# Optimization experiments

Measured on AMD Instinct MI355X. Metric: run time of the kernel, lower is better.

The kernel has to match this reference:

```python
import jax, jax.numpy as jnp
import numpy as np

B = 1_000_000
H = 64
TARGET = 0.62562059 * 10.0  # self.target * scale
# GRN constants from NETC_high.__init__
A1, A2, B1C, B2C, K, NEXP, S, SCALE = 1.0, 1.0, 0.2, 0.2, 1.1, 2, 0.5, 10.0


def setup_inputs() -> dict:
    key = jax.random.key(0)
    ks = jax.random.split(key, 10)
    def xavier(k, shape):
        fan_in, fan_out = shape[1], shape[0]
        std = (2.0 / (fan_in + fan_out)) ** 0.5
        return std * jax.random.normal(k, shape, dtype=jnp.float32)
    return {
        "x": jax.random.uniform(ks[0], (B,), dtype=jnp.float32) * 10.0,
        "y": jax.random.uniform(ks[1], (B,), dtype=jnp.float32) * 10.0,
        "e_x": 0.1 * jax.random.normal(ks[2], (B,), dtype=jnp.float32),
        "e_y": 0.1 * jax.random.normal(ks[3], (B,), dtype=jnp.float32),
        "W1": xavier(ks[4], (H, 2)),
        "b1": jnp.zeros((H,), dtype=jnp.float32),
        "W2": xavier(ks[5], (H, H)),
        "b2": jnp.zeros((H,), dtype=jnp.float32),
        "W3": xavier(ks[6], (1, H)),
        "b3": jnp.zeros((1,), dtype=jnp.float32),
    }


def _mlp(z, W1, b1, W2, b2, W3, b3):
    # ControlNet.function: Linear->ReLU->Linear->ReLU->Linear
    h = jax.nn.relu(z @ W1.T + b1)
    h = jax.nn.relu(h @ W2.T + b2)
    return h @ W3.T + b3  # [*, 1]


def _control(inp, W1, b1, W2, b2, W3, b3):
    # ControlNet.forward: u(x) - u(target)
    tgt = jnp.full((1, 2), TARGET, dtype=inp.dtype)
    return _mlp(inp, W1, b1, W2, b2, W3, b3) - _mlp(tgt, W1, b1, W2, b2, W3, b3)


def reference(x, y, e_x, e_y, W1, b1, W2, b2, W3, b3):
    inp = jnp.stack([x + e_x, y + e_y], axis=-1)  # [B, 2]
    u = _control(inp, W1, b1, W2, b2, W3, b3)[:, 0]  # [B]
    xs = x / SCALE
    ys = y / SCALE
    s2 = S ** NEXP
    hx = xs ** NEXP / (s2 + xs ** NEXP)   # Hill activation in x
    hy = ys ** NEXP / (s2 + ys ** NEXP)
    gx = s2 / (s2 + xs ** NEXP)           # Hill repression by x
    gy = s2 / (s2 + ys ** NEXP)
    dx = SCALE * (A1 * hx + B1C * gy - K * xs + u * hx)
    dy = SCALE * (A2 * hy + B2C * gx - K * ys)
    return (dx, dy, -dx, -dy)
```

## Files before the change

kernel.cpp:

```cpp
#include <hip/hip_runtime.h>

#define BTOT 1000000

typedef _Float16 f16;
typedef f16 f16x2 __attribute__((ext_vector_type(2)));
typedef f16 f16x8 __attribute__((ext_vector_type(8)));
typedef float f32x2 __attribute__((ext_vector_type(2)));
typedef float f32x4 __attribute__((ext_vector_type(4)));

#define WS_BFRAG 16
#define WS_W1A   8208
#define WS_W1B   10256
#define WS_B1P   12304
#define WS_W3V   14352
#define WS_B2V   15376

template<int CTRL>
__device__ __forceinline__ float dpp_add(float v) {
    int pv = __builtin_amdgcn_update_dpp(0, __builtin_bit_cast(int, v),
                                         CTRL, 0xF, 0xF, true);
    return v + __builtin_bit_cast(float, pv);
}
__device__ __forceinline__ float row_reduce16(float p) {
    p = dpp_add<0x128>(p);
    p = dpp_add<0x124>(p);
    p = dpp_add<0x122>(p);
    p = dpp_add<0x121>(p);
    return p;
}

__global__ __launch_bounds__(256) void setup_kernel(
    const float* __restrict__ W1, const float* __restrict__ b1,
    const float* __restrict__ W2, const float* __restrict__ b2,
    const float* __restrict__ W3, unsigned char* __restrict__ ws)
{
    const int tid  = threadIdx.x;
    const int quad = (tid & 63) >> 4;
    const int nl   = tid & 15;

    __shared__ float w2s[64 * 65];
    __shared__ float h1s[64];
    __shared__ float part[4 * 64];

    const float4* W2v = (const float4*)W2;
    #pragma unroll
    for (int r = 0; r < 4; ++r) {
        int idx = r * 256 + tid;
        float4 f = W2v[idx];
        int g = idx * 4, row = g >> 6, col = g & 63;
        float* p = &w2s[row * 65 + col];
        p[0] = f.x; p[1] = f.y; p[2] = f.z; p[3] = f.w;
    }
    const float T = 6.2562059f;
    if (tid < 64)
        h1s[tid] = fmaxf(0.f, W1[2 * tid] * T + W1[2 * tid + 1] * T + b1[tid]);
    __syncthreads();

    {
        int r = tid & 63, kq = tid >> 6;
        float p = 0.f;
        #pragma unroll
        for (int k = 0; k < 16; ++k)
            p = fmaf(w2s[r * 65 + kq * 16 + k], h1s[kq * 16 + k], p);
        part[kq * 64 + r] = p;
    }
    __syncthreads();
    if (tid < 64) {
        float h2 = b2[tid] + part[tid] + part[64 + tid] + part[128 + tid] + part[192 + tid];
        float pr = fmaxf(0.f, h2) * W3[tid];
        #pragma unroll
        for (int m = 1; m < 64; m <<= 1) pr += __shfl_xor(pr, m, 64);
        if (tid == 0) *(float*)ws = pr;
    }

    if (tid < 64) {
        f16x8* bfragT = (f16x8*)(ws + WS_BFRAG);
        #pragma unroll
        for (int n = 0; n < 4; ++n)
            #pragma unroll
            for (int ks = 0; ks < 2; ++ks) {
                f16x8 f;
                #pragma unroll
                for (int j = 0; j < 8; ++j)
                    f[j] = (f16)w2s[(n * 16 + nl) * 65 + ks * 32 + quad * 8 + j];
                bfragT[(n * 2 + ks) * 64 + tid] = f;
            }
        f16x2* w1aT = (f16x2*)(ws + WS_W1A);
        f16x2* w1bT = (f16x2*)(ws + WS_W1B);
        f16x2* b1pT = (f16x2*)(ws + WS_B1P);
        #pragma unroll
        for (int i = 0; i < 8; ++i) {
            int kk = (i < 4) ? (quad * 8 + 2 * i) : (32 + quad * 8 + 2 * (i - 4));
            w1aT[i * 64 + tid] = f16x2{(f16)W1[2 * kk],     (f16)W1[2 * kk + 2]};
            w1bT[i * 64 + tid] = f16x2{(f16)W1[2 * kk + 1], (f16)W1[2 * kk + 3]};
            b1pT[i * 64 + tid] = f16x2{(f16)b1[kk],         (f16)b1[kk + 1]};
        }
        float* w3vT = (float*)(ws + WS_W3V);
        float* b2vT = (float*)(ws + WS_B2V);
        #pragma unroll
        for (int n = 0; n < 4; ++n) {
            w3vT[n * 64 + tid] = W3[n * 16 + nl];
            b2vT[n * 64 + tid] = b2[n * 16 + nl];
        }
    }
}

__global__ __launch_bounds__(256, 4) void netc_kernel(
    const float* __restrict__ x,  const float* __restrict__ y,
    const float* __restrict__ ex, const float* __restrict__ ey,
    const unsigned char* __restrict__ ws,
    float* __restrict__ out)
{
    const int tid  = threadIdx.x;
    const int lane = tid & 63;
    const int wv   = tid >> 6;
    const int quad = lane >> 4;
    const int nl   = lane & 15;

    const float u_tgt = *(const float*)ws;
    const float one_minus_ut = 1.0f - u_tgt;
    const f16x8* bfragT = (const f16x8*)(ws + WS_BFRAG);
    f16x8 bfrag[4][2];
    #pragma unroll
    for (int n = 0; n < 4; ++n)
        #pragma unroll
        for (int ks = 0; ks < 2; ++ks)
            bfrag[n][ks] = bfragT[(n * 2 + ks) * 64 + lane];
    const f16x2* w1aT = (const f16x2*)(ws + WS_W1A);
    const f16x2* w1bT = (const f16x2*)(ws + WS_W1B);
    const f16x2* b1pT = (const f16x2*)(ws + WS_B1P);
    f16x2 w1a[8], w1b[8], b1p[8];
    #pragma unroll
    for (int i = 0; i < 8; ++i) {
        w1a[i] = w1aT[i * 64 + lane];
        w1b[i] = w1bT[i * 64 + lane];
        b1p[i] = b1pT[i * 64 + lane];
    }
    const float* w3vT = (const float*)(ws + WS_W3V);
    const float* b2vT = (const float*)(ws + WS_B2V);
    float w3v[4], b2v[4];
    #pragma unroll
    for (int n = 0; n < 4; ++n) { w3v[n] = w3vT[n * 64 + lane]; b2v[n] = b2vT[n * 64 + lane]; }

    const f16x2 zero2 = {(f16)0.f, (f16)0.f};
    const int nwaves = (gridDim.x * blockDim.x) >> 6;
    const int estep  = nwaves << 6;
    const int srcb = (((nl >> 2) << 4) + quad * 4 + (nl & 3)) << 2;

    int e0 = (((blockIdx.x << 2) + wv) << 6) + lane;

    float axv = 0.f, ayv = 0.f, aexv = 0.f, aeyv = 0.f;
    float bxv = 0.f, byv = 0.f, bexv = 0.f, beyv = 0.f;
    if (e0 < BTOT)         { axv = x[e0]; ayv = y[e0]; aexv = ex[e0]; aeyv = ey[e0]; }
    if (e0 + estep < BTOT) { int p = e0 + estep; bxv = x[p]; byv = y[p]; bexv = ex[p]; beyv = ey[p]; }

    auto body = [&](int ee, float& rx, float& ry, float& rex, float& rey) {
        float cx = rx, cy = ry, cex = rex, cey = rey;
        int pe = ee + 2 * estep;
        if (pe < BTOT) { rx = x[pe]; ry = y[pe]; rex = ex[pe]; rey = ey[pe]; }

        float av = cx + cex, bv = cy + cey;
        f16x2 pab = {(f16)av, (f16)bv};
        int pv = __builtin_bit_cast(int, pab);

        float xs = cx * 0.1f, ys = cy * 0.1f;
        float x2 = xs * xs, y2 = ys * ys;
        float invx = __fdividef(1.0f, 0.25f + x2);
        float invy = __fdividef(1.0f, 0.25f + y2);
        float hx = x2 * invx, hy = y2 * invy;
        float gx = 0.25f * invx, gy = 0.25f * invy;
        float cdx = 10.f * hx;
        float base_dx = fmaf(cdx, one_minus_ut, fmaf(2.f, gy, -11.f * xs));
        float dy = fmaf(10.f, hy, fmaf(2.f, gx, -11.f * ys));
        out[BTOT + ee]     = dy;
        out[3 * BTOT + ee] = -dy;

        f16x2 pt[4];
        #pragma unroll
        for (int t = 0; t < 4; ++t)
            pt[t] = __builtin_bit_cast(f16x2,
                __builtin_amdgcn_ds_bpermute((t * 16 + nl) << 2, pv));

        float ur[4];
        #pragma unroll
        for (int t = 0; t < 4; ++t) {
            f32x4 acc[4];
            #pragma unroll
            for (int n = 0; n < 4; ++n)
                acc[n] = f32x4{b2v[n], b2v[n], b2v[n], b2v[n]};

            f16x2 a2 = {pt[t][0], pt[t][0]};
            f16x2 bb = {pt[t][1], pt[t][1]};
            union { f16x2 h2[8]; f16x8 fr[2]; } u;
            #pragma unroll
            for (int i = 0; i < 8; ++i) {
                f16x2 h = a2 * w1a[i] + (bb * w1b[i] + b1p[i]);
                u.h2[i] = __builtin_elementwise_max(h, zero2);
            }
            #pragma unroll
            for (int n = 0; n < 4; ++n) {
                acc[n] = __builtin_amdgcn_mfma_f32_16x16x32_f16(u.fr[0], bfrag[n][0], acc[n], 0, 0, 0);
                acc[n] = __builtin_amdgcn_mfma_f32_16x16x32_f16(u.fr[1], bfrag[n][1], acc[n], 0, 0, 0);
            }

            f32x2 p01 = {0.f, 0.f}, p23 = {0.f, 0.f};
            #pragma unroll
            for (int n = 0; n < 4; ++n) {
                f32x2 lo = {acc[n][0], acc[n][1]};
                f32x2 hi = {acc[n][2], acc[n][3]};
                lo = __builtin_elementwise_max(lo, f32x2{0.f, 0.f});
                hi = __builtin_elementwise_max(hi, f32x2{0.f, 0.f});
                f32x2 w = {w3v[n], w3v[n]};
                p01 += lo * w;
                p23 += hi * w;
            }
            float u0 = row_reduce16(p01[0]);
            float u1 = row_reduce16(p01[1]);
            float u2 = row_reduce16(p23[0]);
            float u3 = row_reduce16(p23[1]);
            float v01 = (nl & 1) ? u1 : u0;
            float v23 = (nl & 1) ? u3 : u2;
            ur[t] = (nl & 2) ? v23 : v01;
        }

        float s01  = (nl & 4) ? ur[1] : ur[0];
        float s23  = (nl & 4) ? ur[3] : ur[2];
        float send = (nl & 8) ? s23 : s01;
        float u_raw = __builtin_bit_cast(float,
            __builtin_amdgcn_ds_bpermute(srcb, __builtin_bit_cast(int, send)));

        float dx = fmaf(cdx, u_raw, base_dx);
        out[ee]            = dx;
        out[2 * BTOT + ee] = -dx;
    };

    for (int e = e0; e < BTOT; e += 2 * estep) {
        body(e, axv, ayv, aexv, aeyv);
        int e1 = e + estep;
        if (e1 < BTOT)
            body(e1, bxv, byv, bexv, beyv);
    }
}

extern "C" void kernel_launch(void* const* d_in, const int* in_sizes, int n_in,
                              void* d_out, int out_size, void* d_ws, size_t ws_size,
                              hipStream_t stream) {
    const float* x  = (const float*)d_in[0];
    const float* y  = (const float*)d_in[1];
    const float* ex = (const float*)d_in[2];
    const float* ey = (const float*)d_in[3];
    const float* W1 = (const float*)d_in[4];
    const float* b1 = (const float*)d_in[5];
    const float* W2 = (const float*)d_in[6];
    const float* b2 = (const float*)d_in[7];
    const float* W3 = (const float*)d_in[8];
    float* out = (float*)d_out;
    unsigned char* ws = (unsigned char*)d_ws;

    setup_kernel<<<1, 256, 0, stream>>>(W1, b1, W2, b2, W3, ws);
    netc_kernel<<<1024, 256, 0, stream>>>(x, y, ex, ey, ws, out);
}
```

Before: 102.5 us.

## Raise occupancy: single-stage prefetch, 5 blocks per CU, larger grid

```diff
diff --git a/kernel.cpp b/kernel.cpp
--- a/kernel.cpp
+++ b/kernel.cpp
@@ -105,7 +105,7 @@
     }
 }
 
-__global__ __launch_bounds__(256, 4) void netc_kernel(
+__global__ __launch_bounds__(256, 5) void netc_kernel(
     const float* __restrict__ x,  const float* __restrict__ y,
     const float* __restrict__ ex, const float* __restrict__ ey,
     const unsigned char* __restrict__ ws,
@@ -147,17 +147,15 @@
     const int estep  = nwaves << 6;
     const int srcb = (((nl >> 2) << 4) + quad * 4 + (nl & 3)) << 2;
 
-    int e0 = (((blockIdx.x << 2) + wv) << 6) + lane;
-
-    float axv = 0.f, ayv = 0.f, aexv = 0.f, aeyv = 0.f;
-    float bxv = 0.f, byv = 0.f, bexv = 0.f, beyv = 0.f;
-    if (e0 < BTOT)         { axv = x[e0]; ayv = y[e0]; aexv = ex[e0]; aeyv = ey[e0]; }
-    if (e0 + estep < BTOT) { int p = e0 + estep; bxv = x[p]; byv = y[p]; bexv = ex[p]; beyv = ey[p]; }
-
-    auto body = [&](int ee, float& rx, float& ry, float& rex, float& rey) {
-        float cx = rx, cy = ry, cex = rex, cey = rey;
-        int pe = ee + 2 * estep;
-        if (pe < BTOT) { rx = x[pe]; ry = y[pe]; rex = ex[pe]; rey = ey[pe]; }
+    int e = (((blockIdx.x << 2) + wv) << 6) + lane;
+
+    float cx = 0.f, cy = 0.f, cex = 0.f, cey = 0.f;
+    if (e < BTOT) { cx = x[e]; cy = y[e]; cex = ex[e]; cey = ey[e]; }
+
+    for (; e < BTOT; e += estep) {
+        int pe = e + estep;
+        float nx = 0.f, ny = 0.f, nex = 0.f, ney = 0.f;
+        if (pe < BTOT) { nx = x[pe]; ny = y[pe]; nex = ex[pe]; ney = ey[pe]; }
 
         float av = cx + cex, bv = cy + cey;
         f16x2 pab = {(f16)av, (f16)bv};
@@ -172,25 +170,24 @@
         float cdx = 10.f * hx;
         float base_dx = fmaf(cdx, one_minus_ut, fmaf(2.f, gy, -11.f * xs));
         float dy = fmaf(10.f, hy, fmaf(2.f, gx, -11.f * ys));
-        out[BTOT + ee]     = dy;
-        out[3 * BTOT + ee] = -dy;
-
-        f16x2 pt[4];
-        #pragma unroll
-        for (int t = 0; t < 4; ++t)
-            pt[t] = __builtin_bit_cast(f16x2,
+        out[BTOT + e]     = dy;
+        out[3 * BTOT + e] = -dy;
+
+        cx = nx; cy = ny; cex = nex; cey = ney;
+
+        float ur[4];
+        #pragma unroll
+        for (int t = 0; t < 4; ++t) {
+            f16x2 ab = __builtin_bit_cast(f16x2,
                 __builtin_amdgcn_ds_bpermute((t * 16 + nl) << 2, pv));
 
-        float ur[4];
-        #pragma unroll
-        for (int t = 0; t < 4; ++t) {
             f32x4 acc[4];
             #pragma unroll
             for (int n = 0; n < 4; ++n)
                 acc[n] = f32x4{b2v[n], b2v[n], b2v[n], b2v[n]};
 
-            f16x2 a2 = {pt[t][0], pt[t][0]};
-            f16x2 bb = {pt[t][1], pt[t][1]};
+            f16x2 a2 = {ab[0], ab[0]};
+            f16x2 bb = {ab[1], ab[1]};
             union { f16x2 h2[8]; f16x8 fr[2]; } u;
             #pragma unroll
             for (int i = 0; i < 8; ++i) {
@@ -230,15 +227,8 @@
             __builtin_amdgcn_ds_bpermute(srcb, __builtin_bit_cast(int, send)));
 
         float dx = fmaf(cdx, u_raw, base_dx);
-        out[ee]            = dx;
-        out[2 * BTOT + ee] = -dx;
-    };
-
-    for (int e = e0; e < BTOT; e += 2 * estep) {
-        body(e, axv, ayv, aexv, aeyv);
-        int e1 = e + estep;
-        if (e1 < BTOT)
-            body(e1, bxv, byv, bexv, beyv);
+        out[e]            = dx;
+        out[2 * BTOT + e] = -dx;
     }
 }
 
@@ -258,5 +248,5 @@
     unsigned char* ws = (unsigned char*)d_ws;
 
     setup_kernel<<<1, 256, 0, stream>>>(W1, b1, W2, b2, W3, ws);
-    netc_kernel<<<1024, 256, 0, stream>>>(x, y, ex, ey, ws, out);
-}
+    netc_kernel<<<1280, 256, 0, stream>>>(x, y, ex, ey, ws, out);
+}
```

Result: slower. 194.3 us (+89.5%).

## Transpose layer-2 MFMA so weights are A operand and reduce via LDS

Applied to the files above, without the earlier changes.

```diff
diff --git a/kernel.cpp b/kernel.cpp
--- a/kernel.cpp
+++ b/kernel.cpp
@@ -8,26 +8,12 @@
 typedef float f32x2 __attribute__((ext_vector_type(2)));
 typedef float f32x4 __attribute__((ext_vector_type(4)));
 
-#define WS_BFRAG 16
+#define WS_AFRAG 16
 #define WS_W1A   8208
 #define WS_W1B   10256
 #define WS_B1P   12304
-#define WS_W3V   14352
-#define WS_B2V   15376
-
-template<int CTRL>
-__device__ __forceinline__ float dpp_add(float v) {
-    int pv = __builtin_amdgcn_update_dpp(0, __builtin_bit_cast(int, v),
-                                         CTRL, 0xF, 0xF, true);
-    return v + __builtin_bit_cast(float, pv);
-}
-__device__ __forceinline__ float row_reduce16(float p) {
-    p = dpp_add<0x128>(p);
-    p = dpp_add<0x124>(p);
-    p = dpp_add<0x122>(p);
-    p = dpp_add<0x121>(p);
-    return p;
-}
+#define WS_W3Q   14352
+#define WS_B2Q   18448
 
 __global__ __launch_bounds__(256) void setup_kernel(
     const float* __restrict__ W1, const float* __restrict__ b1,
@@ -74,16 +60,16 @@
     }
 
     if (tid < 64) {
-        f16x8* bfragT = (f16x8*)(ws + WS_BFRAG);
-        #pragma unroll
-        for (int n = 0; n < 4; ++n)
+        f16x8* afragT = (f16x8*)(ws + WS_AFRAG);
+        #pragma unroll
+        for (int mt = 0; mt < 4; ++mt)
             #pragma unroll
             for (int ks = 0; ks < 2; ++ks) {
                 f16x8 f;
                 #pragma unroll
                 for (int j = 0; j < 8; ++j)
-                    f[j] = (f16)w2s[(n * 16 + nl) * 65 + ks * 32 + quad * 8 + j];
-                bfragT[(n * 2 + ks) * 64 + tid] = f;
+                    f[j] = (f16)w2s[(mt * 16 + nl) * 65 + ks * 32 + quad * 8 + j];
+                afragT[(mt * 2 + ks) * 64 + tid] = f;
             }
         f16x2* w1aT = (f16x2*)(ws + WS_W1A);
         f16x2* w1bT = (f16x2*)(ws + WS_W1B);
@@ -95,12 +81,13 @@
             w1bT[i * 64 + tid] = f16x2{(f16)W1[2 * kk + 1], (f16)W1[2 * kk + 3]};
             b1pT[i * 64 + tid] = f16x2{(f16)b1[kk],         (f16)b1[kk + 1]};
         }
-        float* w3vT = (float*)(ws + WS_W3V);
-        float* b2vT = (float*)(ws + WS_B2V);
-        #pragma unroll
-        for (int n = 0; n < 4; ++n) {
-            w3vT[n * 64 + tid] = W3[n * 16 + nl];
-            b2vT[n * 64 + tid] = b2[n * 16 + nl];
+        float4* w3q4T = (float4*)(ws + WS_W3Q);
+        float4* b2q4T = (float4*)(ws + WS_B2Q);
+        #pragma unroll
+        for (int mt = 0; mt < 4; ++mt) {
+            int nb = mt * 16 + quad * 4;
+            w3q4T[mt * 64 + tid] = float4{W3[nb], W3[nb + 1], W3[nb + 2], W3[nb + 3]};
+            b2q4T[mt * 64 + tid] = float4{b2[nb], b2[nb + 1], b2[nb + 2], b2[nb + 3]};
         }
     }
 }
@@ -117,15 +104,20 @@
     const int quad = lane >> 4;
     const int nl   = lane & 15;
 
+    __shared__ float red[1024];
+    const int wbase = wv << 8;
+    const int waddr = wbase + (lane << 2);
+    const int rbase = wbase + (nl << 2) + quad;
+
     const float u_tgt = *(const float*)ws;
     const float one_minus_ut = 1.0f - u_tgt;
-    const f16x8* bfragT = (const f16x8*)(ws + WS_BFRAG);
-    f16x8 bfrag[4][2];
-    #pragma unroll
-    for (int n = 0; n < 4; ++n)
+    const f16x8* afragT = (const f16x8*)(ws + WS_AFRAG);
+    f16x8 afrag[4][2];
+    #pragma unroll
+    for (int mt = 0; mt < 4; ++mt)
         #pragma unroll
         for (int ks = 0; ks < 2; ++ks)
-            bfrag[n][ks] = bfragT[(n * 2 + ks) * 64 + lane];
+            afrag[mt][ks] = afragT[(mt * 2 + ks) * 64 + lane];
     const f16x2* w1aT = (const f16x2*)(ws + WS_W1A);
     const f16x2* w1bT = (const f16x2*)(ws + WS_W1B);
     const f16x2* b1pT = (const f16x2*)(ws + WS_B1P);
@@ -136,16 +128,18 @@
         w1b[i] = w1bT[i * 64 + lane];
         b1p[i] = b1pT[i * 64 + lane];
     }
-    const float* w3vT = (const float*)(ws + WS_W3V);
-    const float* b2vT = (const float*)(ws + WS_B2V);
-    float w3v[4], b2v[4];
-    #pragma unroll
-    for (int n = 0; n < 4; ++n) { w3v[n] = w3vT[n * 64 + lane]; b2v[n] = b2vT[n * 64 + lane]; }
+    const f32x4* w3q4T = (const f32x4*)(ws + WS_W3Q);
+    const f32x4* b2q4T = (const f32x4*)(ws + WS_B2Q);
+    f32x4 w3q4[4], b2q4[4];
+    #pragma unroll
+    for (int mt = 0; mt < 4; ++mt) {
+        w3q4[mt] = w3q4T[mt * 64 + lane];
+        b2q4[mt] = b2q4T[mt * 64 + lane];
+    }
 
     const f16x2 zero2 = {(f16)0.f, (f16)0.f};
     const int nwaves = (gridDim.x * blockDim.x) >> 6;
     const int estep  = nwaves << 6;
-    const int srcb = (((nl >> 2) << 4) + quad * 4 + (nl & 3)) << 2;
 
     int e0 = (((blockIdx.x << 2) + wv) << 6) + lane;
 
@@ -175,59 +169,41 @@
         out[BTOT + ee]     = dy;
         out[3 * BTOT + ee] = -dy;
 
-        f16x2 pt[4];
-        #pragma unroll
-        for (int t = 0; t < 4; ++t)
-            pt[t] = __builtin_bit_cast(f16x2,
-                __builtin_amdgcn_ds_bpermute((t * 16 + nl) << 2, pv));
-
-        float ur[4];
-        #pragma unroll
-        for (int t = 0; t < 4; ++t) {
-            f32x4 acc[4];
-            #pragma unroll
-            for (int n = 0; n < 4; ++n)
-                acc[n] = f32x4{b2v[n], b2v[n], b2v[n], b2v[n]};
-
-            f16x2 a2 = {pt[t][0], pt[t][0]};
-            f16x2 bb = {pt[t][1], pt[t][1]};
+        #pragma unroll
+        for (int g = 0; g < 4; ++g) {
+            f16x2 ab = __builtin_bit_cast(f16x2,
+                __builtin_amdgcn_ds_bpermute((g << 6) + (nl << 2), pv));
+
+            f16x2 a2 = {ab[0], ab[0]};
+            f16x2 bb = {ab[1], ab[1]};
             union { f16x2 h2[8]; f16x8 fr[2]; } u;
             #pragma unroll
             for (int i = 0; i < 8; ++i) {
                 f16x2 h = a2 * w1a[i] + (bb * w1b[i] + b1p[i]);
                 u.h2[i] = __builtin_elementwise_max(h, zero2);
             }
-            #pragma unroll
-            for (int n = 0; n < 4; ++n) {
-                acc[n] = __builtin_amdgcn_mfma_f32_16x16x32_f16(u.fr[0], bfrag[n][0], acc[n], 0, 0, 0);
-                acc[n] = __builtin_amdgcn_mfma_f32_16x16x32_f16(u.fr[1], bfrag[n][1], acc[n], 0, 0, 0);
-            }
-
-            f32x2 p01 = {0.f, 0.f}, p23 = {0.f, 0.f};
-            #pragma unroll
-            for (int n = 0; n < 4; ++n) {
-                f32x2 lo = {acc[n][0], acc[n][1]};
-                f32x2 hi = {acc[n][2], acc[n][3]};
-                lo = __builtin_elementwise_max(lo, f32x2{0.f, 0.f});
-                hi = __builtin_elementwise_max(hi, f32x2{0.f, 0.f});
-                f32x2 w = {w3v[n], w3v[n]};
-                p01 += lo * w;
-                p23 += hi * w;
-            }
-            float u0 = row_reduce16(p01[0]);
-            float u1 = row_reduce16(p01[1]);
-            float u2 = row_reduce16(p23[0]);
-            float u3 = row_reduce16(p23[1]);
-            float v01 = (nl & 1) ? u1 : u0;
-            float v23 = (nl & 1) ? u3 : u2;
-            ur[t] = (nl & 2) ? v23 : v01;
+
+            f32x4 acc[4];
+            #pragma unroll
+            for (int mt = 0; mt < 4; ++mt) {
+                acc[mt] = __builtin_amdgcn_mfma_f32_16x16x32_f16(afrag[mt][0], u.fr[0], b2q4[mt], 0, 0, 0);
+                acc[mt] = __builtin_amdgcn_mfma_f32_16x16x32_f16(afrag[mt][1], u.fr[1], acc[mt], 0, 0, 0);
+            }
+
+            f32x2 s01 = {0.f, 0.f}, s23 = {0.f, 0.f};
+            #pragma unroll
+            for (int mt = 0; mt < 4; ++mt) {
+                f32x4 rel = __builtin_elementwise_max(acc[mt], f32x4{0.f, 0.f, 0.f, 0.f});
+                f32x2 lo = {rel[0], rel[1]}, hi = {rel[2], rel[3]};
+                f32x2 wlo = {w3q4[mt][0], w3q4[mt][1]}, whi = {w3q4[mt][2], w3q4[mt][3]};
+                s01 += lo * wlo;
+                s23 += hi * whi;
+            }
+            f32x2 s2 = s01 + s23;
+            red[waddr + g] = s2[0] + s2[1];
         }
 
-        float s01  = (nl & 4) ? ur[1] : ur[0];
-        float s23  = (nl & 4) ? ur[3] : ur[2];
-        float send = (nl & 8) ? s23 : s01;
-        float u_raw = __builtin_bit_cast(float,
-            __builtin_amdgcn_ds_bpermute(srcb, __builtin_bit_cast(int, send)));
+        float u_raw = red[rbase] + red[rbase + 64] + red[rbase + 128] + red[rbase + 192];
 
         float dx = fmaf(cdx, u_raw, base_dx);
         out[ee]            = dx;
```

New measurement: 107.6 us. 1.05x slower.
